# Optimization experiments

Hardware: AMD Instinct MI355X
Metric: run time of the kernel (lower is better)

Reference implementation:

```python
import jax, jax.numpy as jnp
import numpy as np

N_NODES = 50000
N_EDGES = 400000
IN_DIM, HID, OUT_DIM = 24, 256, 12


def _sage_conv(x, src, dst, w_l, b_l, w_r, num_nodes):
    # PyG SAGEConv (aggr='mean', root_weight=True):
    #   out = lin_l(mean_{j in N(i)} x_j) + lin_r(x_i)
    msg = x[src]                                             # [E, H] gather
    s = jax.ops.segment_sum(msg, dst, num_segments=num_nodes)  # [N, H]
    cnt = jax.ops.segment_sum(jnp.ones((src.shape[0],), x.dtype), dst,
                              num_segments=num_nodes)          # [N]
    mean = s / jnp.maximum(cnt, 1.0)[:, None]
    return mean @ w_l + b_l + x @ w_r


def setup_inputs() -> dict:
    key = jax.random.key(0)
    ks = jax.random.split(key, 16)
    sc = 0.05
    inp = {
        "x": jax.random.normal(ks[0], (N_NODES, IN_DIM), jnp.float32),
        "edge_index": jax.random.randint(ks[1], (2, N_EDGES), 0, N_NODES, jnp.int64),
        # encoder: Linear(24,128) ReLU Linear(128,256) ReLU
        "enc_w1": sc * jax.random.normal(ks[2], (IN_DIM, HID // 2), jnp.float32),
        "enc_b1": jnp.zeros((HID // 2,), jnp.float32),
        "enc_w2": sc * jax.random.normal(ks[3], (HID // 2, HID), jnp.float32),
        "enc_b2": jnp.zeros((HID,), jnp.float32),
        # SAGEConv 1 / 2: lin_l (with bias) on aggregated, lin_r (no bias) on root
        "s1_wl": sc * jax.random.normal(ks[4], (HID, HID), jnp.float32),
        "s1_bl": jnp.zeros((HID,), jnp.float32),
        "s1_wr": sc * jax.random.normal(ks[5], (HID, HID), jnp.float32),
        "s2_wl": sc * jax.random.normal(ks[6], (HID, HID), jnp.float32),
        "s2_bl": jnp.zeros((HID,), jnp.float32),
        "s2_wr": sc * jax.random.normal(ks[7], (HID, HID), jnp.float32),
        # readout: Linear(256,128) ReLU Linear(128,12)
        "ro_w1": sc * jax.random.normal(ks[8], (HID, HID // 2), jnp.float32),
        "ro_b1": jnp.zeros((HID // 2,), jnp.float32),
        "ro_w2": sc * jax.random.normal(ks[9], (HID // 2, OUT_DIM), jnp.float32),
        "ro_b2": jnp.zeros((OUT_DIM,), jnp.float32),
    }
    return inp


def reference(x, edge_index, enc_w1, enc_b1, enc_w2, enc_b2,
              s1_wl, s1_bl, s1_wr, s2_wl, s2_bl, s2_wr,
              ro_w1, ro_b1, ro_w2, ro_b2):
    n = x.shape[0]
    src, dst = edge_index[0], edge_index[1]
    # encoder MLP
    h = jax.nn.relu(x @ enc_w1 + enc_b1)
    h = jax.nn.relu(h @ enc_w2 + enc_b2)
    # two SAGE layers with ReLU
    h = jax.nn.relu(_sage_conv(h, src, dst, s1_wl, s1_bl, s1_wr, n))
    h = jax.nn.relu(_sage_conv(h, src, dst, s2_wl, s2_bl, s2_wr, n))
    # readout MLP
    h = jax.nn.relu(h @ ro_w1 + ro_b1)
    return h @ ro_w2 + ro_b2
```

## Files before the change

### kernel.cpp

```cpp
#include <hip/hip_runtime.h>
#include <hip/hip_bf16.h>

#define N_NODES 50000
#define N_EDGES 400000
#define IN_DIM 24
#define HID 256
#define OUT_DIM 12

typedef _Float16 fp16_t;
typedef __attribute__((ext_vector_type(8))) _Float16 half8;
typedef __attribute__((ext_vector_type(4))) float f32x4;

__device__ __forceinline__ void gload_lds16(const void* g, void* l) {
    typedef __attribute__((address_space(3))) unsigned int u32_lds;
    typedef const __attribute__((address_space(1))) unsigned int u32_glb;
    __builtin_amdgcn_global_load_lds((u32_glb*)(unsigned long long)g,
                                     (u32_lds*)(unsigned int)(unsigned long long)l,
                                     16, 0, 0);
}

template<int K, int M, int ROWS>
__global__ __launch_bounds__(M) void lin_enc1(const float* __restrict__ X,
                                              const float* __restrict__ W,
                                              const float* __restrict__ b,
                                              fp16_t* __restrict__ Y, int N) {
    __shared__ float xs[ROWS][K];
    const int row0 = blockIdx.x * ROWS;
    const int tid = threadIdx.x;
    for (int i = tid; i < ROWS * K; i += M) {
        int r = i / K, k = i - r * K;
        int gr = row0 + r;
        xs[r][k] = (gr < N) ? X[(long long)gr * K + k] : 0.f;
    }
    __syncthreads();
    const int j = tid;
    float acc[ROWS];
    float bj = b[j];
#pragma unroll
    for (int r = 0; r < ROWS; ++r) acc[r] = bj;
    for (int k = 0; k < K; ++k) {
        float w = W[k * M + j];
#pragma unroll
        for (int r = 0; r < ROWS; ++r) acc[r] = fmaf(xs[r][k], w, acc[r]);
    }
#pragma unroll
    for (int r = 0; r < ROWS; ++r) {
        int gr = row0 + r;
        if (gr < N) {
            float v = fmaxf(acc[r], 0.f);
            Y[(size_t)gr * M + j] = (fp16_t)v;
        }
    }
}

__global__ __launch_bounds__(256) void wtrans_all(
    const float* __restrict__ enc_w2,
    const float* __restrict__ s1_wl, const float* __restrict__ s1_wr,
    const float* __restrict__ s2_wl, const float* __restrict__ s2_wr,
    const float* __restrict__ ro_w1,
    fp16_t* __restrict__ wtE,
    fp16_t* __restrict__ wtS1,
    fp16_t* __restrict__ wtS2,
    fp16_t* __restrict__ wtR,
    int* __restrict__ deg, int N) {
    const int sE = 256 * 128, sS = 256 * 512, sR = 128 * 256;
    int idx = blockIdx.x * blockDim.x + threadIdx.x;
    if (idx < N) deg[idx] = 0;
    float v; fp16_t* p; int o;
    if (idx < sE) {
        int j = idx / 128, k = idx - j * 128;
        v = enc_w2[(size_t)k * 256 + j]; p = wtE; o = idx;
    } else if (idx < sE + sS) {
        int t = idx - sE; int j = t / 512, k = t - j * 512;
        v = (k < 256) ? s1_wl[(size_t)k * 256 + j] : s1_wr[(size_t)(k - 256) * 256 + j];
        p = wtS1; o = t;
    } else if (idx < sE + 2 * sS) {
        int t = idx - sE - sS; int j = t / 512, k = t - j * 512;
        v = (k < 256) ? s2_wl[(size_t)k * 256 + j] : s2_wr[(size_t)(k - 256) * 256 + j];
        p = wtS2; o = t;
    } else if (idx < sE + 2 * sS + sR) {
        int t = idx - sE - 2 * sS; int j = t / 256, k = t - j * 256;
        v = ro_w1[(size_t)k * 128 + j]; p = wtR; o = t;
    } else return;
    p[o] = (fp16_t)v;
}

template<int K, int MODE, int BM, int BN, bool WH16, bool RELU>
__global__ __launch_bounds__((BM / 64) * (BN / 64) * 64, 4) void gemm_mfma(
    const fp16_t* __restrict__ A, const fp16_t* __restrict__ A2,
    const fp16_t* __restrict__ W,
    const float* __restrict__ bias,
    fp16_t* __restrict__ Yh,
    int N, int M) {
    constexpr int NWR = BM / 64;
    constexpr int NWC = BN / 64;
    constexpr int NT = NWR * NWC * 64;
    __shared__ __align__(16) fp16_t ldsA[BM * 32];
    __shared__ __align__(16) fp16_t ldsB[BN * 32];
    const int tid = threadIdx.x;
    const int r0 = blockIdx.x * BM;
    const int j0 = blockIdx.y * BN;
    const int w = tid >> 6, lane = tid & 63;
    const int wr = w / NWC, wc = w % NWC;
    const int lrow = lane & 15, lg = lane >> 4;

    f32x4 acc[4][4] = {};

    for (int kc = 0; kc < K; kc += 32) {
        __syncthreads();
        const fp16_t* pa;
        int ka, KA;
        if (MODE == 1) {
            KA = HID;
            if (kc >= HID) { pa = A2; ka = kc - HID; }
            else           { pa = A;  ka = kc; }
        } else {
            KA = K; pa = A; ka = kc;
        }
#pragma unroll
        for (int c = tid; c < BM * 4; c += NT) {
            int row = c >> 2, p = c & 3;
            int g = (p - (row >> 1)) & 3;
            int gr = r0 + row; if (gr > N - 1) gr = N - 1;
            gload_lds16(pa + (size_t)gr * KA + ka + g * 8,
                        (char*)ldsA + (size_t)c * 16);
        }
#pragma unroll
        for (int c = tid; c < BN * 4; c += NT) {
            int row = c >> 2, p = c & 3;
            int g = (p - (row >> 1)) & 3;
            gload_lds16(W + (size_t)(j0 + row) * K + kc + g * 8,
                        (char*)ldsB + (size_t)c * 16);
        }
        __syncthreads();

        half8 a[4], b[4];
#pragma unroll
        for (int f = 0; f < 4; ++f) {
            int ar = wr * 64 + f * 16 + lrow;
            int sa = (lg + (ar >> 1)) & 3;
            a[f] = *(const half8*)&ldsA[ar * 32 + sa * 8];
            int br = wc * 64 + f * 16 + lrow;
            int sb = (lg + (br >> 1)) & 3;
            b[f] = *(const half8*)&ldsB[br * 32 + sb * 8];
        }
#pragma unroll
        for (int fi = 0; fi < 4; ++fi)
#pragma unroll
            for (int fj = 0; fj < 4; ++fj)
                acc[fi][fj] = __builtin_amdgcn_mfma_f32_16x16x32_f16(a[fi], b[fj], acc[fi][fj], 0, 0, 0);
    }

#pragma unroll
    for (int fj = 0; fj < 4; ++fj) {
        int ocol = j0 + wc * 64 + fj * 16 + lrow;
        float bv = bias[ocol];
#pragma unroll
        for (int fi = 0; fi < 4; ++fi) {
#pragma unroll
            for (int r = 0; r < 4; ++r) {
                int orow = r0 + wr * 64 + fi * 16 + lg * 4 + r;
                if (orow < N) {
                    float v = acc[fi][fj][r] + bv;
                    if (RELU) v = fmaxf(v, 0.f);
                    if (WH16) Yh[(size_t)orow * M + ocol] = (fp16_t)v;
                }
            }
        }
    }
}

__global__ __launch_bounds__(256, 3) void gemm_ro(
    const fp16_t* __restrict__ A,
    const fp16_t* __restrict__ W,
    const float* __restrict__ b1,
    const float* __restrict__ W2,
    const float* __restrict__ b2,
    float* __restrict__ out, int N) {
    constexpr int K = 256;
    __shared__ __align__(16) fp16_t ldsA[128 * 32];
    __shared__ __align__(16) fp16_t ldsB[128 * 32];
    __shared__ __align__(16) fp16_t htile[128 * 128];
    __shared__ __align__(16) fp16_t w2t[16 * 128];
    const int tid = threadIdx.x;
    const int r0 = blockIdx.x * 128;
    const int w = tid >> 6, lane = tid & 63;
    const int wr = w >> 1, wc = w & 1;
    const int lrow = lane & 15, lg = lane >> 4;

    for (int i = tid; i < 16 * 128; i += 256) {
        int c = i >> 7, k = i & 127;
        w2t[i] = (c < 12) ? (fp16_t)W2[k * 12 + c] : (fp16_t)0.f;
    }

    f32x4 acc[4][4] = {};
    for (int kc = 0; kc < K; kc += 32) {
        __syncthreads();
#pragma unroll
        for (int c = tid; c < 128 * 4; c += 256) {
            int row = c >> 2, p = c & 3;
            int g = (p - (row >> 1)) & 3;
            int gr = r0 + row; if (gr > N - 1) gr = N - 1;
            gload_lds16(A + (size_t)gr * K + kc + g * 8, (char*)ldsA + (size_t)c * 16);
        }
#pragma unroll
        for (int c = tid; c < 128 * 4; c += 256) {
            int row = c >> 2, p = c & 3;
            int g = (p - (row >> 1)) & 3;
            gload_lds16(W + (size_t)row * K + kc + g * 8, (char*)ldsB + (size_t)c * 16);
        }
        __syncthreads();

        half8 a[4], b[4];
#pragma unroll
        for (int f = 0; f < 4; ++f) {
            int ar = wr * 64 + f * 16 + lrow;
            int sa = (lg + (ar >> 1)) & 3;
            a[f] = *(const half8*)&ldsA[ar * 32 + sa * 8];
            int br = wc * 64 + f * 16 + lrow;
            int sb = (lg + (br >> 1)) & 3;
            b[f] = *(const half8*)&ldsB[br * 32 + sb * 8];
        }
#pragma unroll
        for (int fi = 0; fi < 4; ++fi)
#pragma unroll
            for (int fj = 0; fj < 4; ++fj)
                acc[fi][fj] = __builtin_amdgcn_mfma_f32_16x16x32_f16(a[fi], b[fj], acc[fi][fj], 0, 0, 0);
    }

#pragma unroll
    for (int fj = 0; fj < 4; ++fj) {
        int ocol = wc * 64 + fj * 16 + lrow;
        float bv = b1[ocol];
        int q = ocol >> 3;
#pragma unroll
        for (int fi = 0; fi < 4; ++fi) {
#pragma unroll
            for (int r = 0; r < 4; ++r) {
                int orow = wr * 64 + fi * 16 + lg * 4 + r;
                float v = fmaxf(acc[fi][fj][r] + bv, 0.f);
                int phys = (q + (orow >> 1)) & 15;
                htile[orow * 128 + phys * 8 + (ocol & 7)] = (fp16_t)v;
            }
        }
    }
    __syncthreads();

    if (w < 2) {
        f32x4 accF[4] = {};
#pragma unroll
        for (int kt = 0; kt < 4; ++kt) {
            half8 bb = *(const half8*)&w2t[lrow * 128 + kt * 32 + lg * 8];
            half8 a[4];
#pragma unroll
            for (int f = 0; f < 4; ++f) {
                int ar = w * 64 + f * 16 + lrow;
                int q = kt * 4 + lg;
                int phys = (q + (ar >> 1)) & 15;
                a[f] = *(const half8*)&htile[ar * 128 + phys * 8];
            }
#pragma unroll
            for (int f = 0; f < 4; ++f)
                accF[f] = __builtin_amdgcn_mfma_f32_16x16x32_f16(a[f], bb, accF[f], 0, 0, 0);
        }
        if (lrow < OUT_DIM) {
            float bv = b2[lrow];
#pragma unroll
            for (int f = 0; f < 4; ++f) {
#pragma unroll
                for (int r = 0; r < 4; ++r) {
                    int orow = r0 + w * 64 + f * 16 + lg * 4 + r;
                    if (orow < N) out[(size_t)orow * OUT_DIM + lrow] = accF[f][r] + bv;
                }
            }
        }
    }
}

__global__ void deg_kernel(const int* __restrict__ dst, int* __restrict__ deg, int E) {
    int e = blockIdx.x * blockDim.x + threadIdx.x;
    if (e < E) atomicAdd(&deg[dst[e]], 1);
}

__global__ __launch_bounds__(256) void scan_local(const int* __restrict__ deg,
                                                  int* __restrict__ locincl,
                                                  int* __restrict__ bsum, int N) {
    const int t = threadIdx.x;
    const int i = blockIdx.x * 256 + t;
    int v = (i < N) ? deg[i] : 0;
    const int lane = t & 63;
    int x = v;
#pragma unroll
    for (int off = 1; off < 64; off <<= 1) {
        int y = __shfl_up(x, off, 64);
        if (lane >= off) x += y;
    }
    __shared__ int wsum[4];
    if (lane == 63) wsum[t >> 6] = x;
    __syncthreads();
    const int wid = t >> 6;
    int add = 0;
    for (int wI = 0; wI < wid; ++wI) add += wsum[wI];
    x += add;
    if (i < N) locincl[i] = x;
    if (t == 255) bsum[blockIdx.x] = x;
}

__global__ __launch_bounds__(256) void scan_bsum(int* __restrict__ bsum, int B) {
    const int t = threadIdx.x;
    int v = (t < B) ? bsum[t] : 0;
    const int lane = t & 63;
    int x = v;
#pragma unroll
    for (int off = 1; off < 64; off <<= 1) {
        int y = __shfl_up(x, off, 64);
        if (lane >= off) x += y;
    }
    __shared__ int wsum[4];
    if (lane == 63) wsum[t >> 6] = x;
    __syncthreads();
    const int wid = t >> 6;
    int add = 0;
    for (int wI = 0; wI < wid; ++wI) add += wsum[wI];
    x += add;
    if (t < B) bsum[t] = x - v;
}

__global__ __launch_bounds__(256) void scan_final(const int* __restrict__ deg,
                                                  const int* __restrict__ locincl,
                                                  const int* __restrict__ bsum,
                                                  int* __restrict__ rowptr,
                                                  int* __restrict__ cursor, int N, int E) {
    const int i = blockIdx.x * 256 + threadIdx.x;
    if (i < N) {
        int excl = bsum[blockIdx.x] + locincl[i] - deg[i];
        rowptr[i] = excl;
        cursor[i] = excl;
    }
    if (i == 0) rowptr[N] = E;
}

__global__ void scatter_kernel(const int* __restrict__ src, const int* __restrict__ dst,
                               int* __restrict__ cursor, int* __restrict__ esrc, int E) {
    int e = blockIdx.x * blockDim.x + threadIdx.x;
    if (e < E) {
        int pos = atomicAdd(&cursor[dst[e]], 1);
        esrc[pos] = src[e];
    }
}

__global__ __launch_bounds__(256) void agg_csr(const fp16_t* __restrict__ h,
                                               const int* __restrict__ rowptr,
                                               const int* __restrict__ esrc,
                                               fp16_t* __restrict__ mean, int N) {
    const int n = blockIdx.x * 4 + (threadIdx.x >> 6);
    if (n >= N) return;
    const int lane = threadIdx.x & 63;
    const int half = lane >> 5;
    const int l32 = lane & 31;
    const int r0 = rowptr[n];
    const int r1 = rowptr[n + 1];
    const int deg = r1 - r0;

    float acc[8];
#pragma unroll
    for (int j = 0; j < 8; ++j) acc[j] = 0.f;

    for (int e = r0 + half; e < r1; e += 2) {
        int s = esrc[e];
        half8 v = *(const half8*)&h[(size_t)s * HID + l32 * 8];
#pragma unroll
        for (int j = 0; j < 8; ++j) acc[j] += (float)v[j];
    }
#pragma unroll
    for (int j = 0; j < 8; ++j) acc[j] += __shfl(acc[j], lane ^ 32, 64);

    if (half == 0) {
        float inv = 1.0f / fmaxf((float)deg, 1.0f);
        half8 o;
#pragma unroll
        for (int j = 0; j < 8; ++j) o[j] = (fp16_t)(acc[j] * inv);
        *(half8*)&mean[(size_t)n * HID + l32 * 8] = o;
    }
}

extern "C" void kernel_launch(void* const* d_in, const int* in_sizes, int n_in,
                              void* d_out, int out_size, void* d_ws, size_t ws_size,
                              hipStream_t stream) {
    const float* x      = (const float*)d_in[0];
    const int*   eidx   = (const int*)d_in[1];
    const float* enc_w1 = (const float*)d_in[2];
    const float* enc_b1 = (const float*)d_in[3];
    const float* enc_w2 = (const float*)d_in[4];
    const float* enc_b2 = (const float*)d_in[5];
    const float* s1_wl  = (const float*)d_in[6];
    const float* s1_bl  = (const float*)d_in[7];
    const float* s1_wr  = (const float*)d_in[8];
    const float* s2_wl  = (const float*)d_in[9];
    const float* s2_bl  = (const float*)d_in[10];
    const float* s2_wr  = (const float*)d_in[11];
    const float* ro_w1  = (const float*)d_in[12];
    const float* ro_b1  = (const float*)d_in[13];
    const float* ro_w2  = (const float*)d_in[14];
    const float* ro_b2  = (const float*)d_in[15];
    float* out = (float*)d_out;

    const int N = N_NODES;
    const int E = N_EDGES;
    const int* src = eidx;
    const int* dst = eidx + E;

    char* ws = (char*)d_ws;
    size_t off = 0;
    auto alloc = [&](size_t bytes) { void* p = ws + off; off += (bytes + 255) & ~255ULL; return p; };
    int* deg     = (int*)alloc((size_t)N * 4);
    int* rowptr  = (int*)alloc((size_t)(N + 1) * 4);
    int* cursor  = (int*)alloc((size_t)N * 4);
    int* esrc    = (int*)alloc((size_t)E * 4);
    int* locincl = (int*)alloc((size_t)N * 4);
    int* bsum    = (int*)alloc((size_t)256 * 4);
    fp16_t* wtE  = (fp16_t*)alloc((size_t)256 * 128 * 2);
    fp16_t* wtS1 = (fp16_t*)alloc((size_t)256 * 512 * 2);
    fp16_t* wtS2 = (fp16_t*)alloc((size_t)256 * 512 * 2);
    fp16_t* wtR  = (fp16_t*)alloc((size_t)128 * 256 * 2);
    fp16_t* h0   = (fp16_t*)alloc((size_t)N * 128 * 2);
    fp16_t* hA   = (fp16_t*)alloc((size_t)N * HID * 2);
    fp16_t* hB   = (fp16_t*)alloc((size_t)N * HID * 2);
    fp16_t* mbuf = (fp16_t*)alloc((size_t)N * HID * 2);

    const int nb8 = (N + 7) / 8;
    const int gx128 = (N + 127) / 128;
    const int nbScan = (N + 255) / 256;
    const int nbAgg = (N + 3) / 4;
    const int wtTot = 256 * 128 + 2 * 256 * 512 + 128 * 256;

    wtrans_all<<<(wtTot + 255) / 256, 256, 0, stream>>>(
        enc_w2, s1_wl, s1_wr, s2_wl, s2_wr, ro_w1, wtE, wtS1, wtS2, wtR, deg, N);

    deg_kernel<<<(E + 255) / 256, 256, 0, stream>>>(dst, deg, E);
    scan_local<<<nbScan, 256, 0, stream>>>(deg, locincl, bsum, N);
    scan_bsum<<<1, 256, 0, stream>>>(bsum, nbScan);
    scan_final<<<nbScan, 256, 0, stream>>>(deg, locincl, bsum, rowptr, cursor, N, E);
    scatter_kernel<<<(E + 255) / 256, 256, 0, stream>>>(src, dst, cursor, esrc, E);

    lin_enc1<IN_DIM, 128, 8><<<nb8, 128, 0, stream>>>(x, enc_w1, enc_b1, h0, N);
    gemm_mfma<128, 0, 128, 256, true, true><<<dim3(gx128, 1), 512, 0, stream>>>(
        h0, nullptr, wtE, enc_b2, hA, N, 256);

    agg_csr<<<nbAgg, 256, 0, stream>>>(hA, rowptr, esrc, mbuf, N);
    gemm_mfma<512, 1, 128, 256, true, true><<<dim3(gx128, 1), 512, 0, stream>>>(
        mbuf, hA, wtS1, s1_bl, hB, N, 256);

    agg_csr<<<nbAgg, 256, 0, stream>>>(hB, rowptr, esrc, mbuf, N);
    gemm_mfma<512, 1, 128, 256, true, true><<<dim3(gx128, 1), 512, 0, stream>>>(
        mbuf, hB, wtS2, s2_bl, hA, N, 256);

    gemm_ro<<<gx128, 256, 0, stream>>>(hA, wtR, ro_b1, ro_w2, ro_b2, out, N);
}
```

Before: 229.9 us.

## Fuse encoder MLP into one kernel and merge block-sum scan into scan_final

The first encoder linear layer is now computed directly into a swizzled LDS tile, and the second layer's MFMA GEMM runs in the same kernel. This removes the fp16 h0 intermediate round trip through global memory and one launch. Separately, the single-block scan_bsum kernel is dropped: each scan_final block sums the preceding block totals itself with a wave reduction. That saves a serial launch but does redundant reads of bsum in every block.

```diff
diff --git a/kernel.cpp b/kernel.cpp
--- a/kernel.cpp
+++ b/kernel.cpp
@@ -17,40 +17,6 @@
     __builtin_amdgcn_global_load_lds((u32_glb*)(unsigned long long)g,
                                      (u32_lds*)(unsigned int)(unsigned long long)l,
                                      16, 0, 0);
-}
-
-template<int K, int M, int ROWS>
-__global__ __launch_bounds__(M) void lin_enc1(const float* __restrict__ X,
-                                              const float* __restrict__ W,
-                                              const float* __restrict__ b,
-                                              fp16_t* __restrict__ Y, int N) {
-    __shared__ float xs[ROWS][K];
-    const int row0 = blockIdx.x * ROWS;
-    const int tid = threadIdx.x;
-    for (int i = tid; i < ROWS * K; i += M) {
-        int r = i / K, k = i - r * K;
-        int gr = row0 + r;
-        xs[r][k] = (gr < N) ? X[(long long)gr * K + k] : 0.f;
-    }
-    __syncthreads();
-    const int j = tid;
-    float acc[ROWS];
-    float bj = b[j];
-#pragma unroll
-    for (int r = 0; r < ROWS; ++r) acc[r] = bj;
-    for (int k = 0; k < K; ++k) {
-        float w = W[k * M + j];
-#pragma unroll
-        for (int r = 0; r < ROWS; ++r) acc[r] = fmaf(xs[r][k], w, acc[r]);
-    }
-#pragma unroll
-    for (int r = 0; r < ROWS; ++r) {
-        int gr = row0 + r;
-        if (gr < N) {
-            float v = fmaxf(acc[r], 0.f);
-            Y[(size_t)gr * M + j] = (fp16_t)v;
-        }
-    }
 }
 
 __global__ __launch_bounds__(256) void wtrans_all(
@@ -85,6 +51,90 @@
     p[o] = (fp16_t)v;
 }
 
+__global__ __launch_bounds__(512, 4) void enc_fused(
+    const float* __restrict__ X,
+    const float* __restrict__ W1,
+    const float* __restrict__ b1,
+    const fp16_t* __restrict__ W2t,
+    const float* __restrict__ b2,
+    fp16_t* __restrict__ Y,
+    int N) {
+    __shared__ __align__(16) fp16_t h0t[128 * 128];
+    __shared__ __align__(16) char ubuf[16384];
+    float* w1s = (float*)ubuf;
+    fp16_t* ldsB = (fp16_t*)ubuf;
+    const int tid = threadIdx.x;
+    const int r0 = blockIdx.x * 128;
+    const int w = tid >> 6, lane = tid & 63;
+    const int wr = w >> 2, wc = w & 3;
+    const int lrow = lane & 15, lg = lane >> 4;
+
+    for (int i = tid; i < 24 * 128; i += 512) w1s[i] = W1[i];
+    __syncthreads();
+    {
+        const int c = tid & 127;
+        const int rg = tid >> 7;
+        const int q = c >> 3;
+        for (int i = 0; i < 32; ++i) {
+            int r = rg * 32 + i;
+            int gr = r0 + r; if (gr > N - 1) gr = N - 1;
+            float acc = b1[c];
+#pragma unroll
+            for (int k = 0; k < IN_DIM; ++k)
+                acc = fmaf(X[(size_t)gr * IN_DIM + k], w1s[k * 128 + c], acc);
+            acc = fmaxf(acc, 0.f);
+            int phys = (q + (r >> 1)) & 15;
+            h0t[r * 128 + phys * 8 + (c & 7)] = (fp16_t)acc;
+        }
+    }
+
+    f32x4 acc[4][4] = {};
+    for (int kc = 0; kc < 128; kc += 32) {
+        __syncthreads();
+#pragma unroll
+        for (int c = tid; c < 256 * 4; c += 512) {
+            int row = c >> 2, p = c & 3;
+            int g = (p - (row >> 1)) & 3;
+            gload_lds16(W2t + (size_t)row * 128 + kc + g * 8, (char*)ldsB + (size_t)c * 16);
+        }
+        __syncthreads();
+
+        half8 a[4], b[4];
+#pragma unroll
+        for (int f = 0; f < 4; ++f) {
+            int ar = wr * 64 + f * 16 + lrow;
+            int q = (kc >> 3) + lg;
+            int phys = (q + (ar >> 1)) & 15;
+            a[f] = *(const half8*)&h0t[ar * 128 + phys * 8];
+            int br = wc * 64 + f * 16 + lrow;
+            int sb = (lg + (br >> 1)) & 3;
+            b[f] = *(const half8*)&ldsB[br * 32 + sb * 8];
+        }
+#pragma unroll
+        for (int fi = 0; fi < 4; ++fi)
+#pragma unroll
+            for (int fj = 0; fj < 4; ++fj)
+                acc[fi][fj] = __builtin_amdgcn_mfma_f32_16x16x32_f16(a[fi], b[fj], acc[fi][fj], 0, 0, 0);
+    }
+
+#pragma unroll
+    for (int fj = 0; fj < 4; ++fj) {
+        int ocol = wc * 64 + fj * 16 + lrow;
+        float bv = b2[ocol];
+#pragma unroll
+        for (int fi = 0; fi < 4; ++fi) {
+#pragma unroll
+            for (int r = 0; r < 4; ++r) {
+                int orow = r0 + wr * 64 + fi * 16 + lg * 4 + r;
+                if (orow < N) {
+                    float v = fmaxf(acc[fi][fj][r] + bv, 0.f);
+                    Y[(size_t)orow * HID + ocol] = (fp16_t)v;
+                }
+            }
+        }
+    }
+}
+
 template<int K, int MODE, int BM, int BN, bool WH16, bool RELU>
 __global__ __launch_bounds__((BM / 64) * (BN / 64) * 64, 4) void gemm_mfma(
     const fp16_t* __restrict__ A, const fp16_t* __restrict__ A2,
@@ -306,34 +356,23 @@
     if (t == 255) bsum[blockIdx.x] = x;
 }
 
-__global__ __launch_bounds__(256) void scan_bsum(int* __restrict__ bsum, int B) {
-    const int t = threadIdx.x;
-    int v = (t < B) ? bsum[t] : 0;
-    const int lane = t & 63;
-    int x = v;
-#pragma unroll
-    for (int off = 1; off < 64; off <<= 1) {
-        int y = __shfl_up(x, off, 64);
-        if (lane >= off) x += y;
-    }
-    __shared__ int wsum[4];
-    if (lane == 63) wsum[t >> 6] = x;
-    __syncthreads();
-    const int wid = t >> 6;
-    int add = 0;
-    for (int wI = 0; wI < wid; ++wI) add += wsum[wI];
-    x += add;
-    if (t < B) bsum[t] = x - v;
-}
-
 __global__ __launch_bounds__(256) void scan_final(const int* __restrict__ deg,
                                                   const int* __restrict__ locincl,
                                                   const int* __restrict__ bsum,
                                                   int* __restrict__ rowptr,
-                                                  int* __restrict__ cursor, int N, int E) {
-    const int i = blockIdx.x * 256 + threadIdx.x;
+                                                  int* __restrict__ cursor,
+                                                  int N, int E, int B) {
+    __shared__ int red[4];
+    const int t = threadIdx.x;
+    int s = (t < blockIdx.x && t < B) ? bsum[t] : 0;
+#pragma unroll
+    for (int off = 32; off > 0; off >>= 1) s += __shfl_down(s, off, 64);
+    if ((t & 63) == 0) red[t >> 6] = s;
+    __syncthreads();
+    int base = red[0] + red[1] + red[2] + red[3];
+    const int i = blockIdx.x * 256 + t;
     if (i < N) {
-        int excl = bsum[blockIdx.x] + locincl[i] - deg[i];
+        int excl = base + locincl[i] - deg[i];
         rowptr[i] = excl;
         cursor[i] = excl;
     }
@@ -423,12 +462,10 @@
     fp16_t* wtS1 = (fp16_t*)alloc((size_t)256 * 512 * 2);
     fp16_t* wtS2 = (fp16_t*)alloc((size_t)256 * 512 * 2);
     fp16_t* wtR  = (fp16_t*)alloc((size_t)128 * 256 * 2);
-    fp16_t* h0   = (fp16_t*)alloc((size_t)N * 128 * 2);
     fp16_t* hA   = (fp16_t*)alloc((size_t)N * HID * 2);
     fp16_t* hB   = (fp16_t*)alloc((size_t)N * HID * 2);
     fp16_t* mbuf = (fp16_t*)alloc((size_t)N * HID * 2);
 
-    const int nb8 = (N + 7) / 8;
     const int gx128 = (N + 127) / 128;
     const int nbScan = (N + 255) / 256;
     const int nbAgg = (N + 3) / 4;
@@ -439,13 +476,10 @@
 
     deg_kernel<<<(E + 255) / 256, 256, 0, stream>>>(dst, deg, E);
     scan_local<<<nbScan, 256, 0, stream>>>(deg, locincl, bsum, N);
-    scan_bsum<<<1, 256, 0, stream>>>(bsum, nbScan);
-    scan_final<<<nbScan, 256, 0, stream>>>(deg, locincl, bsum, rowptr, cursor, N, E);
+    scan_final<<<nbScan, 256, 0, stream>>>(deg, locincl, bsum, rowptr, cursor, N, E, nbScan);
     scatter_kernel<<<(E + 255) / 256, 256, 0, stream>>>(src, dst, cursor, esrc, E);
 
-    lin_enc1<IN_DIM, 128, 8><<<nb8, 128, 0, stream>>>(x, enc_w1, enc_b1, h0, N);
-    gemm_mfma<128, 0, 128, 256, true, true><<<dim3(gx128, 1), 512, 0, stream>>>(
-        h0, nullptr, wtE, enc_b2, hA, N, 256);
+    enc_fused<<<gx128, 512, 0, stream>>>(x, enc_w1, enc_b1, wtE, enc_b2, hA, N);
 
     agg_csr<<<nbAgg, 256, 0, stream>>>(hA, rowptr, esrc, mbuf, N);
     gemm_mfma<512, 1, 128, 256, true, true><<<dim3(gx128, 1), 512, 0, stream>>>(
```

Measured after the change: 234.8 us. 2.1% more time.
